# Optimization experiments

Measured on AMD Instinct MI355X. Metric: run time of the kernel, lower is better.

## Reference

```python
import jax, jax.numpy as jnp
import numpy as np

B, C, D, K = 2048, 1, 256, 64  # batch, channels, num variables, units per fold
NUM_LEVELS = 8                 # log2(D) levels of (product + sum)


def setup_inputs() -> dict:
    key = jax.random.key(0)
    ks = jax.random.split(key, 2 + 2 * NUM_LEVELS)
    inp = {}
    inp["x"] = jax.random.normal(ks[0], (B, C, D), dtype=jnp.float32)
    # input-layer bookkeeping: fold f reads variable f (scope of size 1)
    inp["scope_idx"] = jnp.arange(D, dtype=jnp.int32)[:, None]           # (D, 1)
    inp["w_in"] = jax.random.normal(ks[1], (D, K, C), dtype=jnp.float32) * 0.1
    F = D
    for l in range(NUM_LEVELS):
        Fo = F // 2
        # irregular fold bookkeeping: random pairing of input folds
        perm = jax.random.permutation(ks[2 + 2 * l], F)
        inp[f"idx{l}"] = perm.reshape(Fo, 2).astype(jnp.int32)           # (Fo, 2)
        inp[f"w{l}"] = (jax.random.normal(ks[3 + 2 * l], (Fo, K, K), dtype=jnp.float32)
                         * np.float32(1.0 / np.sqrt(K)))
        F = Fo
    return inp


def reference(x, scope_idx, w_in, idx0, w0, idx1, w1, idx2, w2, idx3, w3,
              idx4, w4, idx5, w5, idx6, w6, idx7, w7):
    # --- input layers: gather x[..., scope_idx] -> permute(2,1,0,3) -> (F, C, B, S=1)
    z = x[:, :, scope_idx[:, 0]]                      # (B, C, F)
    h = jnp.einsum('bcf,fkc->fbk', z, w_in)           # (F, B, K) linear input layer
    # --- inner layers: per-level gather (fold bookkeeping) + Hadamard + dense sum
    for idx, w in ((idx0, w0), (idx1, w1), (idx2, w2), (idx3, w3),
                   (idx4, w4), (idx5, w5), (idx6, w6), (idx7, w7)):
        g = h[idx]                                    # (Fo, 2, B, K) irregular gather
        p = g[:, 0] * g[:, 1]                         # Hadamard product layer
        h = jnp.einsum('fbi,foi->fbo', p, w)          # folded dense sum layer
    # --- output bookkeeping: single root fold, then transpose(0, 1)
    return jnp.transpose(h, (1, 0, 2))                # (B, 1, K)
```

## Files before the change

### kernel.cpp

```cpp
#include <hip/hip_runtime.h>


#define NTH 256

struct Params {
  const float* x;     const int* scope;  const float* w_in;
  const int* idx0; const float* w0;  const int* idx1; const float* w1;
  const int* idx2; const float* w2;  const int* idx3; const float* w3;
  const int* idx4; const float* w4;  const int* idx5; const float* w5;
  const int* idx6; const float* w6;  const int* idx7; const float* w7;
  float* v4;
  float* out;
  int B;
};

__global__ __launch_bounds__(NTH) void subtree_kernel(Params P) {
  const int g = blockIdx.x, t = threadIdx.x;
  __shared__ int   T[32];
  __shared__ float V[16][64];

  if (t == 0) {
    int A3[2], A2[4], A1[8], A0[16];
    A3[0] = P.idx3[2 * g]; A3[1] = P.idx3[2 * g + 1];
    for (int i = 0; i < 2; ++i) { A2[2*i] = P.idx2[2*A3[i]]; A2[2*i+1] = P.idx2[2*A3[i]+1]; }
    for (int i = 0; i < 4; ++i) { A1[2*i] = P.idx1[2*A2[i]]; A1[2*i+1] = P.idx1[2*A2[i]+1]; }
    for (int i = 0; i < 8; ++i) { A0[2*i] = P.idx0[2*A1[i]]; A0[2*i+1] = P.idx0[2*A1[i]+1]; }
    for (int i = 0; i < 16; ++i) T[i] = A0[i];
    for (int i = 0; i < 8;  ++i) T[16 + i] = A1[i];
    for (int i = 0; i < 4;  ++i) T[24 + i] = A2[i];
    T[28] = A3[0]; T[29] = A3[1]; T[30] = 0; T[31] = 0;
  }
  __syncthreads();

  {
    const int s = t >> 4, k4 = (t & 15) * 4;
    *(float4*)&V[s][k4] = *(const float4*)(P.w_in + (size_t)T[s] * 64 + k4);
  }
  __syncthreads();

  const float* wl[4] = {P.w0, P.w1, P.w2, P.w3};
  const int G = t >> 6, lane = t & 63;
  #pragma unroll
  for (int lev = 0; lev < 4; ++lev) {
    const int nops = 8 >> lev;
    for (int op = G; op < nops; op += 4) {
      const int s0 = op << (lev + 1), s1 = s0 + (1 << lev);
      const int feat = (lev == 0) ? T[16 + op]
                     : (lev == 1) ? T[24 + op]
                     : (lev == 2) ? T[28 + op] : g;
      const float* wp = wl[lev] + (size_t)feat * 4096 + lane * 64;
      float acc = 0.f;
      #pragma unroll
      for (int q = 0; q < 16; ++q) {
        float4 wv = *(const float4*)(wp + 4 * q);
        float4 a  = *(const float4*)&V[s0][4 * q];
        float4 b  = *(const float4*)&V[s1][4 * q];
        acc = fmaf(a.x * b.x, wv.x, acc);
        acc = fmaf(a.y * b.y, wv.y, acc);
        acc = fmaf(a.z * b.z, wv.z, acc);
        acc = fmaf(a.w * b.w, wv.w, acc);
      }
      V[s0][lane] = acc;
    }
    __syncthreads();
  }
  if (t < 64) P.v4[g * 64 + t] = V[0][t];
}

__global__ __launch_bounds__(NTH) void root_kernel(Params P) {
  const int t = threadIdx.x;
  __shared__ float VA[16][64];
  __shared__ float VB[8][64];
  __shared__ float v8[64];

  {
    const int s = t >> 4, k4 = (t & 15) * 4;
    *(float4*)&VA[s][k4] = *(const float4*)(P.v4 + s * 64 + k4);
  }
  __syncthreads();

  const float* wl[4] = {P.w4, P.w5, P.w6, P.w7};
  const int*   il[4] = {P.idx4, P.idx5, P.idx6, P.idx7};
  const int G = t >> 6, lane = t & 63;
  #pragma unroll
  for (int lev = 0; lev < 4; ++lev) {
    const int nops = 8 >> lev;
    for (int op = G; op < nops; op += 4) {
      const int i0 = il[lev][2 * op], i1 = il[lev][2 * op + 1];
      const float* a = (lev & 1) ? VB[i0] : VA[i0];
      const float* b = (lev & 1) ? VB[i1] : VA[i1];
      const float* wp = wl[lev] + (size_t)op * 4096 + lane * 64;
      float acc = 0.f;
      #pragma unroll
      for (int q = 0; q < 16; ++q) {
        float4 wv = *(const float4*)(wp + 4 * q);
        float4 av = *(const float4*)(a + 4 * q);
        float4 bv = *(const float4*)(b + 4 * q);
        acc = fmaf(av.x * bv.x, wv.x, acc);
        acc = fmaf(av.y * bv.y, wv.y, acc);
        acc = fmaf(av.z * bv.z, wv.z, acc);
        acc = fmaf(av.w * bv.w, wv.w, acc);
      }
      float* dst = (lev == 3) ? v8 : ((lev & 1) ? VA[op] : VB[op]);
      dst[lane] = acc;
    }
    __syncthreads();
  }

  const int rows = P.B >> 4;
  const int r = blockIdx.x * rows + (t >> 1);
  const int half = t & 1;
  const float4* xp = (const float4*)(P.x + (size_t)r * 256 + half * 128);
  float p0 = 1.f, p1 = 1.f;
  #pragma unroll
  for (int q = 0; q < 32; q += 2) {
    float4 u = xp[q], v = xp[q + 1];
    p0 *= (u.x * u.y) * (u.z * u.w);
    p1 *= (v.x * v.y) * (v.z * v.w);
  }
  float pr = p0 * p1;
  float other = __shfl_xor(pr, 1);
  float beta = pr * other;
  float4* o4 = (float4*)(P.out + (size_t)r * 64 + half * 32);
  #pragma unroll
  for (int q = 0; q < 8; ++q) {
    float4 v = *(const float4*)&v8[half * 32 + 4 * q];
    o4[q] = make_float4(beta * v.x, beta * v.y, beta * v.z, beta * v.w);
  }
}

extern "C" void kernel_launch(void* const* d_in, const int* in_sizes, int n_in,
                              void* d_out, int out_size, void* d_ws, size_t ws_size,
                              hipStream_t stream) {
  Params P;
  P.x     = (const float*)d_in[0];
  P.scope = (const int*)d_in[1];
  P.w_in  = (const float*)d_in[2];
  P.idx0 = (const int*)d_in[3];  P.w0 = (const float*)d_in[4];
  P.idx1 = (const int*)d_in[5];  P.w1 = (const float*)d_in[6];
  P.idx2 = (const int*)d_in[7];  P.w2 = (const float*)d_in[8];
  P.idx3 = (const int*)d_in[9];  P.w3 = (const float*)d_in[10];
  P.idx4 = (const int*)d_in[11]; P.w4 = (const float*)d_in[12];
  P.idx5 = (const int*)d_in[13]; P.w5 = (const float*)d_in[14];
  P.idx6 = (const int*)d_in[15]; P.w6 = (const float*)d_in[16];
  P.idx7 = (const int*)d_in[17]; P.w7 = (const float*)d_in[18];
  P.B    = in_sizes[0] / 256;
  P.v4   = (float*)d_ws;
  P.out  = (float*)d_out;

  subtree_kernel<<<16, NTH, 0, stream>>>(P);
  root_kernel<<<16, NTH, 0, stream>>>(P);
}
```

Before: 28.38 us.

## Split subtree evaluation into per-level wide kernels and precompute row products separately

The old 16-block subtree kernel evaluated levels 0-3 serially in one block per subtree. It is replaced by three kernels: level 0 over 128 blocks, level 1 over 64 blocks, and levels 2-3 over 16 blocks. Each uses four lanes per output with a shuffle reduction, so the weight reads are spread across many more CUs. The per-row product of x is now computed in extra blocks of the first kernel and stored to workspace. The root kernel then runs on B/32 blocks and only scales the root vector by that stored value. In exchange there are four launches instead of two, intermediates make round trips through global memory, and each root block still recomputes levels 4-7 redundantly.

```diff
diff --git a/kernel.cpp b/kernel.cpp
--- a/kernel.cpp
+++ b/kernel.cpp
@@ -9,65 +9,116 @@
   const int* idx2; const float* w2;  const int* idx3; const float* w3;
   const int* idx4; const float* w4;  const int* idx5; const float* w5;
   const int* idx6; const float* w6;  const int* idx7; const float* w7;
+  float* beta;
+  float* h1;
+  float* h2;
   float* v4;
   float* out;
   int B;
 };
 
-__global__ __launch_bounds__(NTH) void subtree_kernel(Params P) {
-  const int g = blockIdx.x, t = threadIdx.x;
-  __shared__ int   T[32];
-  __shared__ float V[16][64];
+__global__ __launch_bounds__(NTH) void k1_kernel(Params P) {
+  const int t = threadIdx.x;
+  if (blockIdx.x < 128) {
+    const int o = blockIdx.x;
+    const int a = P.idx0[2 * o], b = P.idx0[2 * o + 1];
+    const int oo = t >> 2, q = t & 3;
+    const float4* va4 = (const float4*)(P.w_in + (size_t)a * 64 + q * 16);
+    const float4* vb4 = (const float4*)(P.w_in + (size_t)b * 64 + q * 16);
+    const float4* wv4 = (const float4*)(P.w0 + (size_t)o * 4096 + oo * 64 + q * 16);
+    float acc = 0.f;
+    #pragma unroll
+    for (int e = 0; e < 4; ++e) {
+      float4 va = va4[e], vb = vb4[e], wv = wv4[e];
+      acc = fmaf(va.x * vb.x, wv.x, acc);
+      acc = fmaf(va.y * vb.y, wv.y, acc);
+      acc = fmaf(va.z * vb.z, wv.z, acc);
+      acc = fmaf(va.w * vb.w, wv.w, acc);
+    }
+    acc += __shfl_xor(acc, 1);
+    acc += __shfl_xor(acc, 2);
+    if (q == 0) P.h1[o * 64 + oo] = acc;
+  } else {
+    const int r = (blockIdx.x - 128) * 16 + (t >> 4);
+    const int seg = t & 15;
+    const float4* xp = (const float4*)(P.x + (size_t)r * 256 + seg * 16);
+    float4 u0 = xp[0], u1 = xp[1], u2 = xp[2], u3 = xp[3];
+    float pr = ((u0.x * u0.y) * (u0.z * u0.w)) * ((u1.x * u1.y) * (u1.z * u1.w))
+             * ((u2.x * u2.y) * (u2.z * u2.w)) * ((u3.x * u3.y) * (u3.z * u3.w));
+    pr *= __shfl_xor(pr, 1);
+    pr *= __shfl_xor(pr, 2);
+    pr *= __shfl_xor(pr, 4);
+    pr *= __shfl_xor(pr, 8);
+    if (seg == 0) P.beta[r] = pr;
+  }
+}
 
-  if (t == 0) {
-    int A3[2], A2[4], A1[8], A0[16];
-    A3[0] = P.idx3[2 * g]; A3[1] = P.idx3[2 * g + 1];
-    for (int i = 0; i < 2; ++i) { A2[2*i] = P.idx2[2*A3[i]]; A2[2*i+1] = P.idx2[2*A3[i]+1]; }
-    for (int i = 0; i < 4; ++i) { A1[2*i] = P.idx1[2*A2[i]]; A1[2*i+1] = P.idx1[2*A2[i]+1]; }
-    for (int i = 0; i < 8; ++i) { A0[2*i] = P.idx0[2*A1[i]]; A0[2*i+1] = P.idx0[2*A1[i]+1]; }
-    for (int i = 0; i < 16; ++i) T[i] = A0[i];
-    for (int i = 0; i < 8;  ++i) T[16 + i] = A1[i];
-    for (int i = 0; i < 4;  ++i) T[24 + i] = A2[i];
-    T[28] = A3[0]; T[29] = A3[1]; T[30] = 0; T[31] = 0;
+__global__ __launch_bounds__(NTH) void k2_kernel(Params P) {
+  const int t = threadIdx.x, o = blockIdx.x;
+  const int a = P.idx1[2 * o], b = P.idx1[2 * o + 1];
+  const int oo = t >> 2, q = t & 3;
+  const float4* va4 = (const float4*)(P.h1 + (size_t)a * 64 + q * 16);
+  const float4* vb4 = (const float4*)(P.h1 + (size_t)b * 64 + q * 16);
+  const float4* wv4 = (const float4*)(P.w1 + (size_t)o * 4096 + oo * 64 + q * 16);
+  float acc = 0.f;
+  #pragma unroll
+  for (int e = 0; e < 4; ++e) {
+    float4 va = va4[e], vb = vb4[e], wv = wv4[e];
+    acc = fmaf(va.x * vb.x, wv.x, acc);
+    acc = fmaf(va.y * vb.y, wv.y, acc);
+    acc = fmaf(va.z * vb.z, wv.z, acc);
+    acc = fmaf(va.w * vb.w, wv.w, acc);
+  }
+  acc += __shfl_xor(acc, 1);
+  acc += __shfl_xor(acc, 2);
+  if (q == 0) P.h2[o * 64 + oo] = acc;
+}
+
+__global__ __launch_bounds__(NTH) void k3_kernel(Params P) {
+  const int t = threadIdx.x, g = blockIdx.x;
+  __shared__ float v3[2][64];
+  {
+    const int opq = t >> 7;
+    const int oo = (t >> 1) & 63, h = t & 1;
+    const int aop = P.idx3[2 * g + opq];
+    const int ia = P.idx2[2 * aop], ib = P.idx2[2 * aop + 1];
+    const float4* va4 = (const float4*)(P.h2 + (size_t)ia * 64 + h * 32);
+    const float4* vb4 = (const float4*)(P.h2 + (size_t)ib * 64 + h * 32);
+    const float4* wv4 = (const float4*)(P.w2 + (size_t)aop * 4096 + oo * 64 + h * 32);
+    float acc = 0.f;
+    #pragma unroll
+    for (int e = 0; e < 8; ++e) {
+      float4 va = va4[e], vb = vb4[e], wv = wv4[e];
+      acc = fmaf(va.x * vb.x, wv.x, acc);
+      acc = fmaf(va.y * vb.y, wv.y, acc);
+      acc = fmaf(va.z * vb.z, wv.z, acc);
+      acc = fmaf(va.w * vb.w, wv.w, acc);
+    }
+    acc += __shfl_xor(acc, 1);
+    if (h == 0) v3[opq][oo] = acc;
   }
   __syncthreads();
-
   {
-    const int s = t >> 4, k4 = (t & 15) * 4;
-    *(float4*)&V[s][k4] = *(const float4*)(P.w_in + (size_t)T[s] * 64 + k4);
+    const int oo = t >> 2, q = t & 3;
+    const float4* wv4 = (const float4*)(P.w3 + (size_t)g * 4096 + oo * 64 + q * 16);
+    const float4* va4 = (const float4*)&v3[0][q * 16];
+    const float4* vb4 = (const float4*)&v3[1][q * 16];
+    float acc = 0.f;
+    #pragma unroll
+    for (int e = 0; e < 4; ++e) {
+      float4 va = va4[e], vb = vb4[e], wv = wv4[e];
+      acc = fmaf(va.x * vb.x, wv.x, acc);
+      acc = fmaf(va.y * vb.y, wv.y, acc);
+      acc = fmaf(va.z * vb.z, wv.z, acc);
+      acc = fmaf(va.w * vb.w, wv.w, acc);
+    }
+    acc += __shfl_xor(acc, 1);
+    acc += __shfl_xor(acc, 2);
+    if (q == 0) P.v4[g * 64 + oo] = acc;
   }
-  __syncthreads();
-
-  const float* wl[4] = {P.w0, P.w1, P.w2, P.w3};
-  const int G = t >> 6, lane = t & 63;
-  #pragma unroll
-  for (int lev = 0; lev < 4; ++lev) {
-    const int nops = 8 >> lev;
-    for (int op = G; op < nops; op += 4) {
-      const int s0 = op << (lev + 1), s1 = s0 + (1 << lev);
-      const int feat = (lev == 0) ? T[16 + op]
-                     : (lev == 1) ? T[24 + op]
-                     : (lev == 2) ? T[28 + op] : g;
-      const float* wp = wl[lev] + (size_t)feat * 4096 + lane * 64;
-      float acc = 0.f;
-      #pragma unroll
-      for (int q = 0; q < 16; ++q) {
-        float4 wv = *(const float4*)(wp + 4 * q);
-        float4 a  = *(const float4*)&V[s0][4 * q];
-        float4 b  = *(const float4*)&V[s1][4 * q];
-        acc = fmaf(a.x * b.x, wv.x, acc);
-        acc = fmaf(a.y * b.y, wv.y, acc);
-        acc = fmaf(a.z * b.z, wv.z, acc);
-        acc = fmaf(a.w * b.w, wv.w, acc);
-      }
-      V[s0][lane] = acc;
-    }
-    __syncthreads();
-  }
-  if (t < 64) P.v4[g * 64 + t] = V[0][t];
 }
 
-__global__ __launch_bounds__(NTH) void root_kernel(Params P) {
+__global__ __launch_bounds__(NTH) void k4_kernel(Params P) {
   const int t = threadIdx.x;
   __shared__ float VA[16][64];
   __shared__ float VB[8][64];
@@ -92,10 +143,10 @@
       const float* wp = wl[lev] + (size_t)op * 4096 + lane * 64;
       float acc = 0.f;
       #pragma unroll
-      for (int q = 0; q < 16; ++q) {
-        float4 wv = *(const float4*)(wp + 4 * q);
-        float4 av = *(const float4*)(a + 4 * q);
-        float4 bv = *(const float4*)(b + 4 * q);
+      for (int qq = 0; qq < 16; ++qq) {
+        float4 wv = *(const float4*)(wp + 4 * qq);
+        float4 av = *(const float4*)(a + 4 * qq);
+        float4 bv = *(const float4*)(b + 4 * qq);
         acc = fmaf(av.x * bv.x, wv.x, acc);
         acc = fmaf(av.y * bv.y, wv.y, acc);
         acc = fmaf(av.z * bv.z, wv.z, acc);
@@ -107,26 +158,14 @@
     __syncthreads();
   }
 
-  const int rows = P.B >> 4;
-  const int r = blockIdx.x * rows + (t >> 1);
-  const int half = t & 1;
-  const float4* xp = (const float4*)(P.x + (size_t)r * 256 + half * 128);
-  float p0 = 1.f, p1 = 1.f;
-  #pragma unroll
-  for (int q = 0; q < 32; q += 2) {
-    float4 u = xp[q], v = xp[q + 1];
-    p0 *= (u.x * u.y) * (u.z * u.w);
-    p1 *= (v.x * v.y) * (v.z * v.w);
-  }
-  float pr = p0 * p1;
-  float other = __shfl_xor(pr, 1);
-  float beta = pr * other;
-  float4* o4 = (float4*)(P.out + (size_t)r * 64 + half * 32);
-  #pragma unroll
-  for (int q = 0; q < 8; ++q) {
-    float4 v = *(const float4*)&v8[half * 32 + 4 * q];
-    o4[q] = make_float4(beta * v.x, beta * v.y, beta * v.z, beta * v.w);
-  }
+  const int r = blockIdx.x * 32 + (t >> 3);
+  const int c0 = (t & 7) * 8;
+  const float be = P.beta[r];
+  float4 a = *(const float4*)&v8[c0];
+  float4 b = *(const float4*)&v8[c0 + 4];
+  float4* o4 = (float4*)(P.out + (size_t)r * 64 + c0);
+  o4[0] = make_float4(be * a.x, be * a.y, be * a.z, be * a.w);
+  o4[1] = make_float4(be * b.x, be * b.y, be * b.z, be * b.w);
 }
 
 extern "C" void kernel_launch(void* const* d_in, const int* in_sizes, int n_in,
@@ -145,9 +184,15 @@
   P.idx6 = (const int*)d_in[15]; P.w6 = (const float*)d_in[16];
   P.idx7 = (const int*)d_in[17]; P.w7 = (const float*)d_in[18];
   P.B    = in_sizes[0] / 256;
-  P.v4   = (float*)d_ws;
+  float* ws = (float*)d_ws;
+  P.beta = ws;
+  P.h1   = ws + 2048;
+  P.h2   = P.h1 + 128 * 64;
+  P.v4   = P.h2 + 64 * 64;
   P.out  = (float*)d_out;
 
-  subtree_kernel<<<16, NTH, 0, stream>>>(P);
-  root_kernel<<<16, NTH, 0, stream>>>(P);
+  k1_kernel<<<256, NTH, 0, stream>>>(P);
+  k2_kernel<<<64,  NTH, 0, stream>>>(P);
+  k3_kernel<<<16,  NTH, 0, stream>>>(P);
+  k4_kernel<<<P.B / 32, NTH, 0, stream>>>(P);
 }
```

Result: faster. 26.38 us (-7.0%).

## Spread subtree, beta product and weight prefetch across many blocks in two kernels

Applied to the files above, without the earlier changes.

The first kernel now runs three roles by block index. Blocks 0-15 compute the level 0-3 subtrees with more threads per level via split-K shuffles. Blocks 16-143 compute the per-row product of x into a workspace. The remaining blocks prefetch the w4-w7 weights into cache. The second kernel is widened to 256 blocks, each redoing the root levels 4-7 and scaling 8 output rows. This is meant to fix the low parallelism of the old 16-block launches and the serial single-thread index chase. The cost is root work duplicated across 256 blocks and an extra workspace round trip for beta.

```diff
diff --git a/kernel.cpp b/kernel.cpp
--- a/kernel.cpp
+++ b/kernel.cpp
@@ -9,73 +9,163 @@
   const int* idx2; const float* w2;  const int* idx3; const float* w3;
   const int* idx4; const float* w4;  const int* idx5; const float* w5;
   const int* idx6; const float* w6;  const int* idx7; const float* w7;
-  float* v4;
-  float* out;
-  int B;
+  float* v4g;
+  float* betag;
+  float* out;  int B;
 };
 
-__global__ __launch_bounds__(NTH) void subtree_kernel(Params P) {
-  const int g = blockIdx.x, t = threadIdx.x;
-  __shared__ int   T[32];
-  __shared__ float V[16][64];
-
-  if (t == 0) {
-    int A3[2], A2[4], A1[8], A0[16];
-    A3[0] = P.idx3[2 * g]; A3[1] = P.idx3[2 * g + 1];
-    for (int i = 0; i < 2; ++i) { A2[2*i] = P.idx2[2*A3[i]]; A2[2*i+1] = P.idx2[2*A3[i]+1]; }
-    for (int i = 0; i < 4; ++i) { A1[2*i] = P.idx1[2*A2[i]]; A1[2*i+1] = P.idx1[2*A2[i]+1]; }
-    for (int i = 0; i < 8; ++i) { A0[2*i] = P.idx0[2*A1[i]]; A0[2*i+1] = P.idx0[2*A1[i]+1]; }
-    for (int i = 0; i < 16; ++i) T[i] = A0[i];
-    for (int i = 0; i < 8;  ++i) T[16 + i] = A1[i];
-    for (int i = 0; i < 4;  ++i) T[24 + i] = A2[i];
-    T[28] = A3[0]; T[29] = A3[1]; T[30] = 0; T[31] = 0;
-  }
-  __syncthreads();
-
-  {
-    const int s = t >> 4, k4 = (t & 15) * 4;
-    *(float4*)&V[s][k4] = *(const float4*)(P.w_in + (size_t)T[s] * 64 + k4);
-  }
-  __syncthreads();
-
-  const float* wl[4] = {P.w0, P.w1, P.w2, P.w3};
-  const int G = t >> 6, lane = t & 63;
-  #pragma unroll
-  for (int lev = 0; lev < 4; ++lev) {
-    const int nops = 8 >> lev;
-    for (int op = G; op < nops; op += 4) {
-      const int s0 = op << (lev + 1), s1 = s0 + (1 << lev);
-      const int feat = (lev == 0) ? T[16 + op]
-                     : (lev == 1) ? T[24 + op]
-                     : (lev == 2) ? T[28 + op] : g;
-      const float* wp = wl[lev] + (size_t)feat * 4096 + lane * 64;
-      float acc = 0.f;
+__device__ inline void sinkf4(float4 v) {
+  asm volatile("" :: "v"(v.x), "v"(v.y), "v"(v.z), "v"(v.w));
+}
+__device__ inline void sinki4(int4 v) {
+  asm volatile("" :: "v"(v.x), "v"(v.y), "v"(v.z), "v"(v.w));
+}
+__device__ inline float dotp(float4 w, float4 a, float4 b, float acc) {
+  acc = fmaf(a.x * b.x, w.x, acc);
+  acc = fmaf(a.y * b.y, w.y, acc);
+  acc = fmaf(a.z * b.z, w.z, acc);
+  acc = fmaf(a.w * b.w, w.w, acc);
+  return acc;
+}
+
+__global__ __launch_bounds__(NTH) void ka_kernel(Params P) {
+  const int t = threadIdx.x, bid = blockIdx.x;
+
+  if (bid < 16) {
+    const int g = bid;
+    __shared__ int   T[32];
+    __shared__ float V0[16][64];
+    __shared__ float L0[8][64];
+    __shared__ float L1[4][64];
+    __shared__ float L2[2][64];
+
+    if (t < 64)       sinki4(((const int4*)P.idx0)[t]);
+    else if (t < 96)  sinki4(((const int4*)P.idx1)[t - 64]);
+    else if (t < 112) sinki4(((const int4*)P.idx2)[t - 96]);
+    else if (t < 120) sinki4(((const int4*)P.idx3)[t - 112]);
+
+    if (t < 2)  T[28 + t] = P.idx3[2 * g + t];
+    __syncthreads();
+    if (t < 4)  T[24 + t] = P.idx2[2 * T[28 + (t >> 1)] + (t & 1)];
+    __syncthreads();
+    if (t < 8)  T[16 + t] = P.idx1[2 * T[24 + (t >> 1)] + (t & 1)];
+    __syncthreads();
+    if (t < 16) T[t]      = P.idx0[2 * T[16 + (t >> 1)] + (t & 1)];
+    __syncthreads();
+
+    {
+      const int s = t >> 4, k4 = (t & 15) * 4;
+      *(float4*)&V0[s][k4] = *(const float4*)(P.w_in + (size_t)T[s] * 64 + k4);
+    }
+    __syncthreads();
+
+    {
+      const int op = t >> 5, tt = t & 31;
+      const float* w = P.w0 + (size_t)T[16 + op] * 4096;
+      const float* a = V0[2 * op];
+      const float* b = V0[2 * op + 1];
+      float acc0 = 0.f, acc1 = 0.f;
       #pragma unroll
       for (int q = 0; q < 16; ++q) {
-        float4 wv = *(const float4*)(wp + 4 * q);
-        float4 a  = *(const float4*)&V[s0][4 * q];
-        float4 b  = *(const float4*)&V[s1][4 * q];
-        acc = fmaf(a.x * b.x, wv.x, acc);
-        acc = fmaf(a.y * b.y, wv.y, acc);
-        acc = fmaf(a.z * b.z, wv.z, acc);
-        acc = fmaf(a.w * b.w, wv.w, acc);
+        float4 av = *(const float4*)(a + 4 * q);
+        float4 bv = *(const float4*)(b + 4 * q);
+        float4 w0v = *(const float4*)(w + (size_t)tt * 64 + 4 * q);
+        float4 w1v = *(const float4*)(w + (size_t)(tt + 32) * 64 + 4 * q);
+        acc0 = dotp(w0v, av, bv, acc0);
+        acc1 = dotp(w1v, av, bv, acc1);
       }
-      V[s0][lane] = acc;
-    }
-    __syncthreads();
-  }
-  if (t < 64) P.v4[g * 64 + t] = V[0][t];
-}
-
-__global__ __launch_bounds__(NTH) void root_kernel(Params P) {
-  const int t = threadIdx.x;
+      L0[op][tt] = acc0;
+      L0[op][tt + 32] = acc1;
+    }
+    __syncthreads();
+
+    {
+      const int op = t >> 6, oo = t & 63;
+      const float* w = P.w1 + (size_t)T[24 + op] * 4096 + (size_t)oo * 64;
+      const float* a = L0[2 * op];
+      const float* b = L0[2 * op + 1];
+      float acc = 0.f;
+      #pragma unroll
+      for (int q = 0; q < 16; ++q)
+        acc = dotp(*(const float4*)(w + 4 * q), *(const float4*)(a + 4 * q),
+                   *(const float4*)(b + 4 * q), acc);
+      L1[op][oo] = acc;
+    }
+    __syncthreads();
+
+    {
+      const int op = t >> 7, tt = t & 127, oo = tt >> 1, q0 = (tt & 1) * 32;
+      const float* w = P.w2 + (size_t)T[28 + op] * 4096 + (size_t)oo * 64 + q0;
+      const float* a = &L1[2 * op][q0];
+      const float* b = &L1[2 * op + 1][q0];
+      float acc = 0.f;
+      #pragma unroll
+      for (int q = 0; q < 8; ++q)
+        acc = dotp(*(const float4*)(w + 4 * q), *(const float4*)(a + 4 * q),
+                   *(const float4*)(b + 4 * q), acc);
+      acc += __shfl_xor(acc, 1);
+      if ((tt & 1) == 0) L2[op][oo] = acc;
+    }
+    __syncthreads();
+
+    {
+      const int oo = t >> 2, q0 = (t & 3) * 16;
+      const float* w = P.w3 + (size_t)g * 4096 + (size_t)oo * 64 + q0;
+      const float* a = &L2[0][q0];
+      const float* b = &L2[1][q0];
+      float acc = 0.f;
+      #pragma unroll
+      for (int q = 0; q < 4; ++q)
+        acc = dotp(*(const float4*)(w + 4 * q), *(const float4*)(a + 4 * q),
+                   *(const float4*)(b + 4 * q), acc);
+      acc += __shfl_xor(acc, 1);
+      acc += __shfl_xor(acc, 2);
+      if ((t & 3) == 0) P.v4g[g * 64 + oo] = acc;
+    }
+  } else if (bid < 144) {
+    const int r = (bid - 16) * 16 + (t >> 4);
+    const int seg = t & 15;
+    const float4* xp = (const float4*)(P.x + (size_t)r * 256 + seg * 16);
+    float4 u0 = xp[0], u1 = xp[1], u2 = xp[2], u3 = xp[3];
+    float pr = ((u0.x * u0.y) * (u0.z * u0.w)) * ((u1.x * u1.y) * (u1.z * u1.w))
+             * ((u2.x * u2.y) * (u2.z * u2.w)) * ((u3.x * u3.y) * (u3.z * u3.w));
+    pr *= __shfl_xor(pr, 1);
+    pr *= __shfl_xor(pr, 2);
+    pr *= __shfl_xor(pr, 4);
+    pr *= __shfl_xor(pr, 8);
+    if (seg == 0) P.betag[r] = pr;
+  } else {
+    auto pref_slice = [&](int s) {
+      const int base = s * 3840;
+      #pragma unroll
+      for (int i = t * 4; i < 3840; i += NTH * 4) {
+        const int fi = base + i;
+        const float* p;
+        if (fi < 32768)       p = P.w4 + fi;
+        else if (fi < 49152)  p = P.w5 + (fi - 32768);
+        else if (fi < 57344)  p = P.w6 + (fi - 49152);
+        else                  p = P.w7 + (fi - 57344);
+        sinkf4(*(const float4*)p);
+      }
+    };
+    const int s = (bid - 144) >> 3;
+    pref_slice(s);
+    if (s < 2) pref_slice(s + 14);
+  }
+}
+
+__global__ __launch_bounds__(NTH) void kb_kernel(Params P) {
+  const int t = threadIdx.x, bid = blockIdx.x;
   __shared__ float VA[16][64];
   __shared__ float VB[8][64];
   __shared__ float v8[64];
-
-  {
-    const int s = t >> 4, k4 = (t & 15) * 4;
-    *(float4*)&VA[s][k4] = *(const float4*)(P.v4 + s * 64 + k4);
+  __shared__ float beta_s[8];
+
+  if (t < 8) beta_s[t] = P.betag[bid * 8 + t];
+  #pragma unroll
+  for (int rr = 0; rr < 4; ++rr) {
+    const int idx = rr * 256 + t;
+    VA[rr * 4 + (t >> 6)][idx & 63] = P.v4g[idx];
   }
   __syncthreads();
 
@@ -92,40 +182,21 @@
       const float* wp = wl[lev] + (size_t)op * 4096 + lane * 64;
       float acc = 0.f;
       #pragma unroll
-      for (int q = 0; q < 16; ++q) {
-        float4 wv = *(const float4*)(wp + 4 * q);
-        float4 av = *(const float4*)(a + 4 * q);
-        float4 bv = *(const float4*)(b + 4 * q);
-        acc = fmaf(av.x * bv.x, wv.x, acc);
-        acc = fmaf(av.y * bv.y, wv.y, acc);
-        acc = fmaf(av.z * bv.z, wv.z, acc);
-        acc = fmaf(av.w * bv.w, wv.w, acc);
-      }
+      for (int qq = 0; qq < 16; ++qq)
+        acc = dotp(*(const float4*)(wp + 4 * qq), *(const float4*)(a + 4 * qq),
+                   *(const float4*)(b + 4 * qq), acc);
       float* dst = (lev == 3) ? v8 : ((lev & 1) ? VA[op] : VB[op]);
       dst[lane] = acc;
     }
     __syncthreads();
   }
 
-  const int rows = P.B >> 4;
-  const int r = blockIdx.x * rows + (t >> 1);
-  const int half = t & 1;
-  const float4* xp = (const float4*)(P.x + (size_t)r * 256 + half * 128);
-  float p0 = 1.f, p1 = 1.f;
-  #pragma unroll
-  for (int q = 0; q < 32; q += 2) {
-    float4 u = xp[q], v = xp[q + 1];
-    p0 *= (u.x * u.y) * (u.z * u.w);
-    p1 *= (v.x * v.y) * (v.z * v.w);
-  }
-  float pr = p0 * p1;
-  float other = __shfl_xor(pr, 1);
-  float beta = pr * other;
-  float4* o4 = (float4*)(P.out + (size_t)r * 64 + half * 32);
-  #pragma unroll
-  for (int q = 0; q < 8; ++q) {
-    float4 v = *(const float4*)&v8[half * 32 + 4 * q];
-    o4[q] = make_float4(beta * v.x, beta * v.y, beta * v.z, beta * v.w);
+  {
+    const int row = t >> 5, c0 = (t & 31) * 2;
+    const float be = beta_s[row];
+    float2 v = *(const float2*)&v8[c0];
+    *(float2*)(P.out + (size_t)(bid * 8 + row) * 64 + c0) =
+        make_float2(be * v.x, be * v.y);
   }
 }
 
@@ -145,9 +216,11 @@
   P.idx6 = (const int*)d_in[15]; P.w6 = (const float*)d_in[16];
   P.idx7 = (const int*)d_in[17]; P.w7 = (const float*)d_in[18];
   P.B    = in_sizes[0] / 256;
-  P.v4   = (float*)d_ws;
-  P.out  = (float*)d_out;
-
-  subtree_kernel<<<16, NTH, 0, stream>>>(P);
-  root_kernel<<<16, NTH, 0, stream>>>(P);
-}
+  float* ws = (float*)d_ws;
+  P.v4g   = ws;
+  P.betag = ws + 16 * 64;
+  P.out   = (float*)d_out;
+
+  ka_kernel<<<256, NTH, 0, stream>>>(P);
+  kb_kernel<<<256, NTH, 0, stream>>>(P);
+}
```

Result: faster. 25.44 us (-10.3%).
